# Performance work log

Measured on AMD Instinct MI355X. Metric: run time of the kernel, lower is better.

## Reference

```python
import jax, jax.numpy as jnp
import numpy as np

N = 100000      # nodes
E = 300000      # directed edges (avg degree ~3, ogbn-arxiv-like sparsity)
F_IN = 128      # ogbn-arxiv node features
H = 256         # hidden
C = 40          # ogbn-arxiv classes
L = 6           # num_layers
BN_EPS = 1e-5


def setup_inputs() -> dict:
    key = jax.random.key(0)
    ks = jax.random.split(key, 12)
    x = jax.random.normal(ks[0], (N, F_IN), jnp.float32)
    edge_index = jax.random.randint(ks[1], (2, E), 0, N, dtype=jnp.int32)
    s_in = 1.0 / np.sqrt(F_IN)
    s_h = 1.0 / np.sqrt(H)
    return {
        "x": x,
        "edge_index": edge_index,
        "w_in": jax.random.normal(ks[2], (F_IN, H), jnp.float32) * s_in,
        "b_in": jnp.zeros((H,), jnp.float32),
        "conv_w": jax.random.normal(ks[3], (L, H, H), jnp.float32) * s_h,
        "conv_b": jnp.zeros((L, H), jnp.float32),
        "bn_gamma": jnp.ones((L, H), jnp.float32),
        "bn_beta": jnp.zeros((L, H), jnp.float32),
        "out_w": jax.random.normal(ks[4], (H, C), jnp.float32) * s_h,
        "out_b": jnp.zeros((C,), jnp.float32),
        "res_weights": jax.random.normal(ks[5], (L,), jnp.float32),
    }


def _gcn_norm(edge_index, n_nodes):
    # GCNConv default: add self-loops, symmetric normalization D^-1/2 (A+I) D^-1/2
    loops = jnp.arange(n_nodes, dtype=edge_index.dtype)
    src = jnp.concatenate([edge_index[0], loops])
    dst = jnp.concatenate([edge_index[1], loops])
    deg = jax.ops.segment_sum(jnp.ones_like(dst, jnp.float32), dst, num_segments=n_nodes)
    dinv = jax.lax.rsqrt(jnp.maximum(deg, 1.0))
    norm = dinv[src] * dinv[dst]  # [E+N]
    return src, dst, norm


def _batchnorm(h, gamma, beta):
    # BatchNorm1d in training mode: biased batch statistics over nodes
    m = jnp.mean(h, axis=0)
    v = jnp.mean(jnp.square(h - m), axis=0)
    return (h - m) * jax.lax.rsqrt(v + BN_EPS) * gamma + beta


def reference(x, edge_index, w_in, b_in, conv_w, conv_b, bn_gamma, bn_beta, out_w, out_b, res_weights):
    src, dst, norm = _gcn_norm(edge_index, N)
    h = x @ w_in + b_in            # input_fc: [N, H]
    x_input = h
    layer_out = []
    prev = None
    for i in range(L):
        hw = h @ conv_w[i]                                  # linear transform
        msg = hw[src] * norm[:, None]                       # gather + scale
        agg = jax.ops.segment_sum(msg, dst, num_segments=N) + conv_b[i]  # scatter-add
        a = jax.nn.relu(_batchnorm(agg, bn_gamma[i], bn_beta[i]))
        # dropout p=0.5 omitted (eval mode / deterministic reference)
        if i == 0:
            h = a + 0.2 * x_input
        else:
            h = a + 0.2 * x_input + 0.7 * prev
        layer_out.append(h)
        prev = h
    w = jax.nn.softmax(res_weights)                          # [L]
    mix = jnp.einsum('lnh,l->nh', jnp.stack(layer_out), w)   # weighted sum of layer outputs
    logits = mix @ out_w + out_b                             # [N, C]
    return jax.nn.log_softmax(logits, axis=1)
```

## Files before the change

kernel.cpp:

```cpp
#include <hip/hip_runtime.h>
#include <math.h>

#define Nn   100000
#define Ee   300000
#define FIN  128
#define Hdim 256
#define Ncls 40
#define Lnum 6
#define SCAN_B 98
#define KP   264
#define EMAX 1152

typedef __attribute__((ext_vector_type(8))) short bf16x8;
typedef __attribute__((ext_vector_type(4))) float f32x4;

__device__ __forceinline__ float bf2f(unsigned int u16) {
    unsigned int x = u16 << 16;
    return __builtin_bit_cast(float, x);
}
__device__ __forceinline__ unsigned short f2bf(float f) {
    unsigned int x = __builtin_bit_cast(unsigned int, f);
    x = (x + 0x7FFFu + ((x >> 16) & 1u)) >> 16;
    return (unsigned short)x;
}
__device__ __forceinline__ void unpack2(unsigned int u, float& lo, float& hi) {
    lo = __builtin_bit_cast(float, u << 16);
    hi = __builtin_bit_cast(float, u & 0xFFFF0000u);
}
__device__ __forceinline__ unsigned int pack2(float a, float b) {
    return (unsigned int)f2bf(a) | ((unsigned int)f2bf(b) << 16);
}
__device__ __forceinline__ void acc8(float* a, float w, uint4 v) {
    float f0, f1;
    unpack2(v.x, f0, f1); a[0] += w * f0; a[1] += w * f1;
    unpack2(v.y, f0, f1); a[2] += w * f0; a[3] += w * f1;
    unpack2(v.z, f0, f1); a[4] += w * f0; a[5] += w * f1;
    unpack2(v.w, f0, f1); a[6] += w * f0; a[7] += w * f1;
}

__global__ void count_edges(const int* __restrict__ ei, int* __restrict__ cnt) {
    int e = blockIdx.x * blockDim.x + threadIdx.x;
    if (e < Ee) atomicAdd(&cnt[ei[Ee + e]], 1);
}

__global__ void scan_block(const int* __restrict__ cnt, int* __restrict__ iscan,
                           int* __restrict__ btot) {
    __shared__ int buf[1024];
    int t = threadIdx.x;
    int g = blockIdx.x * 1024 + t;
    int v = (g < Nn) ? cnt[g] : 0;
    buf[t] = v; __syncthreads();
    for (int off = 1; off < 1024; off <<= 1) {
        int x = buf[t];
        int a = (t >= off) ? buf[t - off] : 0;
        __syncthreads();
        buf[t] = x + a;
        __syncthreads();
    }
    if (g < Nn) iscan[g] = buf[t];
    if (t == 1023) btot[blockIdx.x] = buf[1023];
}

__global__ void scan_tops(const int* __restrict__ btot, int* __restrict__ bpref) {
    __shared__ int b[128];
    int t = threadIdx.x;
    int v = (t < SCAN_B) ? btot[t] : 0;
    b[t] = v; __syncthreads();
    for (int off = 1; off < 128; off <<= 1) {
        int x = b[t];
        int a = (t >= off) ? b[t - off] : 0;
        __syncthreads();
        b[t] = x + a;
        __syncthreads();
    }
    if (t < SCAN_B) bpref[t] = b[t] - v;
}

__global__ void scan_final(const int* __restrict__ cnt, const int* __restrict__ iscan,
                           const int* __restrict__ bpref, int* __restrict__ offs,
                           float* __restrict__ dinvp) {
    int g = blockIdx.x * 1024 + threadIdx.x;
    if (g < Nn) {
        int c = cnt[g];
        offs[g] = bpref[blockIdx.x] + iscan[g] - c;
        dinvp[g] = rsqrtf((float)(c + 1));
    }
    if (g == 0) offs[Nn] = Ee;
}

__global__ void fill_csr(const int* __restrict__ ei, const int* __restrict__ offs,
                         int* __restrict__ cur, const float* __restrict__ dinvp,
                         int* __restrict__ esrc, float* __restrict__ ew) {
    int e = blockIdx.x * blockDim.x + threadIdx.x;
    if (e >= Ee) return;
    int s = ei[e], d = ei[Ee + e];
    int p = offs[d] + atomicAdd(&cur[d], 1);
    esrc[p] = s;
    ew[p] = dinvp[s];
}

__global__ void prep_weights(const float* __restrict__ conv_w, const float* __restrict__ w_in,
                             const float* __restrict__ out_w,
                             unsigned short* __restrict__ Whi,
                             unsigned short* __restrict__ Fhi,
                             unsigned short* __restrict__ Whd, unsigned short* __restrict__ Wld) {
    int b = blockIdx.x, t = threadIdx.x;
    if (b < 1536) {
        int id = b * 256 + t;
        int l = id >> 16, k = (id >> 8) & 255, n = id & 255;
        Whi[l * 65536 + n * 256 + k] = f2bf(conv_w[id]);
    } else if (b < 1664) {
        int id = (b - 1536) * 256 + t;
        int k = id >> 8, n = id & 255;
        Fhi[n * FIN + k] = f2bf(w_in[id]);
    } else {
        int id = (b - 1664) * 256 + t;
        int c = id >> 8, k = id & 255;
        float w = (c < Ncls) ? out_w[k * Ncls + c] : 0.f;
        unsigned short hi = f2bf(w);
        unsigned short lo = f2bf(w - bf2f(hi));
        Whd[c * 256 + k] = hi;
        Wld[c * 256 + k] = lo;
    }
}

__global__ void cvt_bf16(const float* __restrict__ src, unsigned short* __restrict__ dst, int n8) {
    int i = blockIdx.x * blockDim.x + threadIdx.x;
    if (i >= n8) return;
    float4 a = ((const float4*)src)[i * 2];
    float4 b = ((const float4*)src)[i * 2 + 1];
    uint4 o;
    o.x = pack2(a.x, a.y); o.y = pack2(a.z, a.w);
    o.z = pack2(b.x, b.y); o.w = pack2(b.z, b.w);
    ((uint4*)dst)[i] = o;
}

__global__ void bn_reduce(const float* __restrict__ P, float* __restrict__ bnsum,
                          float* __restrict__ bnsq, int nb) {
    int c = threadIdx.x;
    int per = (nb + gridDim.x - 1) / gridDim.x;
    int r0 = blockIdx.x * per;
    int r1 = r0 + per; if (r1 > nb) r1 = nb;
    float s = 0.f, q = 0.f;
    for (int r = r0; r < r1; ++r) {
        s += P[(size_t)r * 512 + c];
        q += P[(size_t)r * 512 + 256 + c];
    }
    if (r0 < r1) {
        atomicAdd(&bnsum[c], s);
        atomicAdd(&bnsq[c], q);
    }
}

__global__ __launch_bounds__(512) void gemm_mfma(
    const unsigned short* __restrict__ A, unsigned short* __restrict__ C,
    const unsigned short* __restrict__ W,
    const float* __restrict__ bias, int K, int nrows)
{
    __shared__ __align__(16) unsigned short smem[18432];

    const int t    = threadIdx.x;
    const int lane = t & 63, wid = t >> 6;
    const int ln   = lane & 15, quad = lane >> 4;
    const int r64  = (wid >> 2) * 64, c64 = (wid & 3) * 64;
    const int r0   = blockIdx.x * 128;

    unsigned short* At = smem;
    unsigned short* Bt = smem + 5120;

    f32x4 acc[4][4];
#pragma unroll
    for (int i = 0; i < 4; ++i)
#pragma unroll
        for (int j = 0; j < 4; ++j) acc[i][j] = (f32x4){0.f, 0.f, 0.f, 0.f};

    const int arow = t >> 2, akq = t & 3;
    const bool arow_ok = (r0 + arow < nrows);
    const int nk = K >> 5;

    uint4 ga = make_uint4(0u, 0u, 0u, 0u);
    if (arow_ok) ga = *(const uint4*)&A[(size_t)(r0 + arow) * K + akq * 8];
    uint4 gb[2];
#pragma unroll
    for (int q = 0; q < 2; ++q) {
        int idx = t + 512 * q, row = idx >> 2, kq = idx & 3;
        gb[q] = *(const uint4*)&W[(size_t)row * K + kq * 8];
    }

    for (int kt = 0; kt < nk; ++kt) {
        __syncthreads();
        *(uint4*)&At[arow * 40 + akq * 8] = ga;
#pragma unroll
        for (int q = 0; q < 2; ++q) {
            int idx = t + 512 * q, row = idx >> 2, kq = idx & 3;
            *(uint4*)&Bt[row * 40 + kq * 8] = gb[q];
        }
        __syncthreads();
        if (kt + 1 < nk) {
            int k0 = (kt + 1) << 5;
            ga = make_uint4(0u, 0u, 0u, 0u);
            if (arow_ok) ga = *(const uint4*)&A[(size_t)(r0 + arow) * K + k0 + akq * 8];
#pragma unroll
            for (int q = 0; q < 2; ++q) {
                int idx = t + 512 * q, row = idx >> 2, kq = idx & 3;
                gb[q] = *(const uint4*)&W[(size_t)row * K + k0 + kq * 8];
            }
        }
        bf16x8 af[4], bf[4];
#pragma unroll
        for (int rt = 0; rt < 4; ++rt)
            af[rt] = *(const bf16x8*)&At[(r64 + rt * 16 + ln) * 40 + quad * 8];
#pragma unroll
        for (int ct = 0; ct < 4; ++ct)
            bf[ct] = *(const bf16x8*)&Bt[(c64 + ct * 16 + ln) * 40 + quad * 8];
#pragma unroll
        for (int rt = 0; rt < 4; ++rt)
#pragma unroll
            for (int ct = 0; ct < 4; ++ct)
                acc[rt][ct] = __builtin_amdgcn_mfma_f32_16x16x32_bf16(af[rt], bf[ct], acc[rt][ct], 0, 0, 0);
    }
    __syncthreads();

    float bc[4];
#pragma unroll
    for (int ct = 0; ct < 4; ++ct) bc[ct] = bias[c64 + ct * 16 + ln];

    unsigned short* Tt = &smem[wid * 2304];
    const int rr2 = lane & 31, jh = lane >> 5;
#pragma unroll
    for (int h = 0; h < 2; ++h) {
#pragma unroll
        for (int rr = 0; rr < 2; ++rr) {
            int rt = 2 * h + rr;
#pragma unroll
            for (int ct = 0; ct < 4; ++ct)
#pragma unroll
                for (int v = 0; v < 4; ++v)
                    Tt[(rr * 16 + quad * 4 + v) * 72 + ct * 16 + ln] = f2bf(acc[rt][ct][v] + bc[ct]);
        }
        __asm__ volatile("s_waitcnt lgkmcnt(0)" ::: "memory");
        int grow = r0 + r64 + h * 32 + rr2;
        if (grow < nrows) {
#pragma unroll
            for (int j = 0; j < 4; ++j) {
                uint4 v4 = *(const uint4*)&Tt[rr2 * 72 + jh * 32 + j * 8];
                *(uint4*)&C[(size_t)grow * 256 + c64 + jh * 32 + j * 8] = v4;
            }
        }
        __asm__ volatile("s_waitcnt lgkmcnt(0)" ::: "memory");
    }
}

__global__ __launch_bounds__(512, 4) void gemm_agg(
    const unsigned short* __restrict__ Hin,
    unsigned short* __restrict__ C,
    const unsigned short* __restrict__ W,
    const float* __restrict__ bias,
    const int* __restrict__ offs, const int* __restrict__ esrc,
    const float* __restrict__ ew, const float* __restrict__ dinvp,
    float* __restrict__ bnsum, float* __restrict__ bnsq,
    float* __restrict__ Pstats)
{
    __shared__ __align__(16) unsigned short At[128 * KP];
    __shared__ __align__(16) uint2 eL[EMAX];
    __shared__ int oL[132];
    __shared__ float lsum[256], lsq[256];

    const int t    = threadIdx.x;
    const int lane = t & 63, wid = t >> 6;
    const int ln   = lane & 15, quad = lane >> 4;
    const int r64  = (wid >> 2) * 64, c64 = (wid & 3) * 64;
    const int r0   = blockIdx.x * 128;

    if (t < 256) { lsum[t] = 0.f; lsq[t] = 0.f; }

    const int rEnd = (r0 + 128 <= Nn) ? (r0 + 128) : Nn;
    const int E0 = offs[r0];
    const int E1 = offs[rEnd];
    const int nE = E1 - E0;
    const bool staged = (nE <= EMAX);

    if (t < 129) {
        int idx = r0 + t; if (idx > Nn) idx = Nn;
        oL[t] = offs[idx];
    }
    if (staged) {
        for (int j = t; j < nE; j += 512)
            eL[j] = make_uint2((unsigned)esrc[E0 + j],
                               __builtin_bit_cast(unsigned, ew[E0 + j]));
    }
    __syncthreads();

    const int half = lane >> 5, l31 = lane & 31;
#pragma unroll 1
    for (int p = 0; p < 4; ++p) {
        const int rA = (wid * 2 + half) * 8 + 2 * p, rB = rA + 1;
        const int nA = r0 + rA, nB = r0 + rB;
        float a[8] = {0.f,0.f,0.f,0.f,0.f,0.f,0.f,0.f};
        float b[8] = {0.f,0.f,0.f,0.f,0.f,0.f,0.f,0.f};
        int eA = oL[rA], eA1 = oL[rA + 1];
        int eB = oL[rB], eB1 = oL[rB + 1];
        float dnA = 0.f, dnB = 0.f;
        if (nA < Nn) {
            dnA = dinvp[nA];
            acc8(a, dnA, *(const uint4*)&Hin[(size_t)nA * Hdim + l31 * 8]);
        }
        if (nB < Nn) {
            dnB = dinvp[nB];
            acc8(b, dnB, *(const uint4*)&Hin[(size_t)nB * Hdim + l31 * 8]);
        }
        if (staged) {
            bool dA = eA < eA1, dB = eB < eB1;
            uint4 vA = make_uint4(0u,0u,0u,0u), vB = vA;
            float wA = 0.f, wB = 0.f;
            if (dA) { uint2 s = eL[eA - E0]; wA = __builtin_bit_cast(float, s.y);
                      vA = *(const uint4*)&Hin[(size_t)s.x * Hdim + l31 * 8]; }
            if (dB) { uint2 s = eL[eB - E0]; wB = __builtin_bit_cast(float, s.y);
                      vB = *(const uint4*)&Hin[(size_t)s.x * Hdim + l31 * 8]; }
            while (dA | dB) {
                bool dA2 = dA && (eA + 1 < eA1), dB2 = dB && (eB + 1 < eB1);
                uint4 vA2 = make_uint4(0u,0u,0u,0u), vB2 = vA2;
                float wA2 = 0.f, wB2 = 0.f;
                if (dA2) { uint2 s = eL[eA + 1 - E0]; wA2 = __builtin_bit_cast(float, s.y);
                           vA2 = *(const uint4*)&Hin[(size_t)s.x * Hdim + l31 * 8]; }
                if (dB2) { uint2 s = eL[eB + 1 - E0]; wB2 = __builtin_bit_cast(float, s.y);
                           vB2 = *(const uint4*)&Hin[(size_t)s.x * Hdim + l31 * 8]; }
                if (dA) { acc8(a, wA, vA); ++eA; }
                if (dB) { acc8(b, wB, vB); ++eB; }
                vA = vA2; wA = wA2; dA = dA2;
                vB = vB2; wB = wB2; dB = dB2;
            }
        } else {
            for (int e = eA; e < eA1; ++e) {
                int s = esrc[e]; float w = ew[e];
                acc8(a, w, *(const uint4*)&Hin[(size_t)s * Hdim + l31 * 8]);
            }
            for (int e = eB; e < eB1; ++e) {
                int s = esrc[e]; float w = ew[e];
                acc8(b, w, *(const uint4*)&Hin[(size_t)s * Hdim + l31 * 8]);
            }
        }
#pragma unroll
        for (int k = 0; k < 8; ++k) { a[k] *= dnA; b[k] *= dnB; }
        *(uint4*)&At[rA * KP + l31 * 8] =
            make_uint4(pack2(a[0], a[1]), pack2(a[2], a[3]),
                       pack2(a[4], a[5]), pack2(a[6], a[7]));
        *(uint4*)&At[rB * KP + l31 * 8] =
            make_uint4(pack2(b[0], b[1]), pack2(b[2], b[3]),
                       pack2(b[4], b[5]), pack2(b[6], b[7]));
    }
    __syncthreads();

    f32x4 acc[4][4];
#pragma unroll
    for (int i = 0; i < 4; ++i)
#pragma unroll
        for (int j = 0; j < 4; ++j) acc[i][j] = (f32x4){0.f, 0.f, 0.f, 0.f};

#pragma unroll
    for (int kt = 0; kt < 8; ++kt) {
        bf16x8 af[4], bf[4];
#pragma unroll
        for (int ct = 0; ct < 4; ++ct)
            bf[ct] = *(const bf16x8*)&W[(size_t)(c64 + ct * 16 + ln) * 256 + kt * 32 + quad * 8];
#pragma unroll
        for (int rt = 0; rt < 4; ++rt)
            af[rt] = *(const bf16x8*)&At[(r64 + rt * 16 + ln) * KP + kt * 32 + quad * 8];
#pragma unroll
        for (int rt = 0; rt < 4; ++rt)
#pragma unroll
            for (int ct = 0; ct < 4; ++ct)
                acc[rt][ct] = __builtin_amdgcn_mfma_f32_16x16x32_bf16(af[rt], bf[ct], acc[rt][ct], 0, 0, 0);
    }

    float bc[4];
#pragma unroll
    for (int ct = 0; ct < 4; ++ct) bc[ct] = bias[c64 + ct * 16 + ln];

#pragma unroll
    for (int ct = 0; ct < 4; ++ct) {
        float s = 0.f, qq = 0.f;
#pragma unroll
        for (int rt = 0; rt < 4; ++rt)
#pragma unroll
            for (int v = 0; v < 4; ++v) {
                int row = r0 + r64 + rt * 16 + quad * 4 + v;
                if (row < Nn) {
                    float val = acc[rt][ct][v] + bc[ct];
                    s += val; qq += val * val;
                }
            }
        s  += __shfl_xor(s, 16);  s  += __shfl_xor(s, 32);
        qq += __shfl_xor(qq, 16); qq += __shfl_xor(qq, 32);
        if (quad == 0) { atomicAdd(&lsum[c64 + ct * 16 + ln], s); atomicAdd(&lsq[c64 + ct * 16 + ln], qq); }
    }

    __syncthreads();

#pragma unroll
    for (int rt = 0; rt < 4; ++rt)
#pragma unroll
        for (int ct = 0; ct < 4; ++ct)
#pragma unroll
            for (int v = 0; v < 4; ++v)
                At[(r64 + rt * 16 + quad * 4 + v) * KP + c64 + ct * 16 + ln] =
                    f2bf(acc[rt][ct][v] + bc[ct]);
    __syncthreads();

    const int l31s = t & 31, rhalf = t >> 5;
#pragma unroll
    for (int p = 0; p < 8; ++p) {
        int lrow = p * 16 + rhalf;
        int grow = r0 + lrow;
        if (grow < Nn) {
            uint4 v4 = *(const uint4*)&At[lrow * KP + l31s * 8];
            *(uint4*)&C[(size_t)grow * 256 + l31s * 8] = v4;
        }
    }

    if (t < 256) {
        if (Pstats) {
            Pstats[(size_t)blockIdx.x * 512 + t]       = lsum[t];
            Pstats[(size_t)blockIdx.x * 512 + 256 + t] = lsq[t];
        } else {
            atomicAdd(&bnsum[t], lsum[t]);
            atomicAdd(&bnsq[t], lsq[t]);
        }
    }
}

__global__ void apply_kernel(const unsigned short* __restrict__ T,
                             const unsigned short* __restrict__ X,
                             unsigned short* __restrict__ Hb, unsigned short* __restrict__ M,
                             const float* __restrict__ bnsum, const float* __restrict__ bnsq,
                             const float* __restrict__ gamma, const float* __restrict__ beta,
                             const float* __restrict__ res_w, int layer) {
    __shared__ float sc[256], sh[256];
    int t = threadIdx.x;
    {
        float mean = bnsum[t] * (1.0f / Nn);
        float var  = fmaxf(bnsq[t] * (1.0f / Nn) - mean * mean, 0.f);
        float rstd = rsqrtf(var + 1e-5f);
        float s = gamma[t] * rstd;
        sc[t] = s; sh[t] = beta[t] - mean * s;
    }
    float m0 = res_w[0];
#pragma unroll
    for (int i = 1; i < Lnum; ++i) m0 = fmaxf(m0, res_w[i]);
    float se = 0.f, wl = 0.f;
#pragma unroll
    for (int i = 0; i < Lnum; ++i) {
        float e = __expf(res_w[i] - m0);
        se += e;
        if (i == layer) wl = e;
    }
    float wi = wl / se;
    __syncthreads();

    int idx = blockIdx.x * blockDim.x + t;
    int c8 = idx & 31;
    float scl[8], shl[8];
#pragma unroll
    for (int k = 0; k < 8; ++k) { scl[k] = sc[c8 * 8 + k]; shl[k] = sh[c8 * 8 + k]; }

    uint4 tv = ((const uint4*)T)[idx];
    uint4 xv = ((const uint4*)X)[idx];
    float tf[8], xf[8];
    unpack2(tv.x, tf[0], tf[1]); unpack2(tv.y, tf[2], tf[3]);
    unpack2(tv.z, tf[4], tf[5]); unpack2(tv.w, tf[6], tf[7]);
    unpack2(xv.x, xf[0], xf[1]); unpack2(xv.y, xf[2], xf[3]);
    unpack2(xv.z, xf[4], xf[5]); unpack2(xv.w, xf[6], xf[7]);

    float a[8];
#pragma unroll
    for (int k = 0; k < 8; ++k)
        a[k] = fmaxf(tf[k] * scl[k] + shl[k], 0.f) + 0.2f * xf[k];
    if (layer > 0) {
        uint4 hv = ((const uint4*)Hb)[idx];
        float hf[8];
        unpack2(hv.x, hf[0], hf[1]); unpack2(hv.y, hf[2], hf[3]);
        unpack2(hv.z, hf[4], hf[5]); unpack2(hv.w, hf[6], hf[7]);
#pragma unroll
        for (int k = 0; k < 8; ++k) a[k] += 0.7f * hf[k];
    }
    uint4 ho;
    ho.x = pack2(a[0], a[1]); ho.y = pack2(a[2], a[3]);
    ho.z = pack2(a[4], a[5]); ho.w = pack2(a[6], a[7]);
    ((uint4*)Hb)[idx] = ho;

    float m[8];
    if (layer == 0) {
#pragma unroll
        for (int k = 0; k < 8; ++k) m[k] = wi * a[k];
    } else {
        uint4 mv = ((const uint4*)M)[idx];
        float mf[8];
        unpack2(mv.x, mf[0], mf[1]); unpack2(mv.y, mf[2], mf[3]);
        unpack2(mv.z, mf[4], mf[5]); unpack2(mv.w, mf[6], mf[7]);
#pragma unroll
        for (int k = 0; k < 8; ++k) m[k] = mf[k] + wi * a[k];
    }
    uint4 mo;
    mo.x = pack2(m[0], m[1]); mo.y = pack2(m[2], m[3]);
    mo.z = pack2(m[4], m[5]); mo.w = pack2(m[6], m[7]);
    ((uint4*)M)[idx] = mo;
}

__global__ __launch_bounds__(512) void head_mfma(const unsigned short* __restrict__ M,
                                                 const unsigned short* __restrict__ Whd,
                                                 const unsigned short* __restrict__ Wld,
                                                 const float* __restrict__ out_b,
                                                 float* __restrict__ out, int nrows) {
    __shared__ unsigned short At[128 * 40];
    const int t    = threadIdx.x;
    const int lane = t & 63, wid = t >> 6;
    const int ln   = lane & 15, quad = lane >> 4;
    const int r0   = blockIdx.x * 128;

    f32x4 acc[3];
#pragma unroll
    for (int ct = 0; ct < 3; ++ct) acc[ct] = (f32x4){0.f, 0.f, 0.f, 0.f};

    for (int k0 = 0; k0 < 256; k0 += 32) {
        __syncthreads();
        {
            int row = t >> 2, kq = t & 3;
            uint4 g = make_uint4(0u, 0u, 0u, 0u);
            if (r0 + row < nrows)
                g = *(const uint4*)&M[(size_t)(r0 + row) * 256 + k0 + kq * 8];
            *(uint4*)&At[row * 40 + kq * 8] = g;
        }
        __syncthreads();
        bf16x8 af = *(const bf16x8*)&At[(wid * 16 + ln) * 40 + quad * 8];
#pragma unroll
        for (int ct = 0; ct < 3; ++ct) {
            int c = ct * 16 + ln;
            bf16x8 bh = *(const bf16x8*)&Whd[c * 256 + k0 + quad * 8];
            bf16x8 bl = *(const bf16x8*)&Wld[c * 256 + k0 + quad * 8];
            acc[ct] = __builtin_amdgcn_mfma_f32_16x16x32_bf16(af, bh, acc[ct], 0, 0, 0);
            acc[ct] = __builtin_amdgcn_mfma_f32_16x16x32_bf16(af, bl, acc[ct], 0, 0, 0);
        }
    }

    int   cc[3]; float bias[3];
#pragma unroll
    for (int ct = 0; ct < 3; ++ct) {
        cc[ct] = ct * 16 + ln;
        bias[ct] = (cc[ct] < Ncls) ? out_b[cc[ct]] : 0.f;
    }
#pragma unroll
    for (int v = 0; v < 4; ++v) {
        int row = r0 + wid * 16 + quad * 4 + v;
        float val[3];
#pragma unroll
        for (int ct = 0; ct < 3; ++ct) val[ct] = acc[ct][v] + bias[ct];
        float mx = -1e30f;
#pragma unroll
        for (int ct = 0; ct < 3; ++ct) if (cc[ct] < Ncls) mx = fmaxf(mx, val[ct]);
        mx = fmaxf(mx, __shfl_xor(mx, 1)); mx = fmaxf(mx, __shfl_xor(mx, 2));
        mx = fmaxf(mx, __shfl_xor(mx, 4)); mx = fmaxf(mx, __shfl_xor(mx, 8));
        float s = 0.f;
#pragma unroll
        for (int ct = 0; ct < 3; ++ct) if (cc[ct] < Ncls) s += __expf(val[ct] - mx);
        s += __shfl_xor(s, 1); s += __shfl_xor(s, 2);
        s += __shfl_xor(s, 4); s += __shfl_xor(s, 8);
        float lse = mx + __logf(s);
        if (row < nrows) {
            out[(size_t)row * Ncls + cc[0]] = val[0] - lse;
            out[(size_t)row * Ncls + cc[1]] = val[1] - lse;
            if (ln < 8) out[(size_t)row * Ncls + cc[2]] = val[2] - lse;
        }
    }
}

extern "C" void kernel_launch(void* const* d_in, const int* in_sizes, int n_in,
                              void* d_out, int out_size, void* d_ws, size_t ws_size,
                              hipStream_t stream)
{
    const float* x      = (const float*)d_in[0];
    const int*   ei     = (const int*)d_in[1];
    const float* w_in   = (const float*)d_in[2];
    const float* b_in   = (const float*)d_in[3];
    const float* conv_w = (const float*)d_in[4];
    const float* conv_b = (const float*)d_in[5];
    const float* gamma  = (const float*)d_in[6];
    const float* beta   = (const float*)d_in[7];
    const float* out_w  = (const float*)d_in[8];
    const float* out_b  = (const float*)d_in[9];
    const float* res_w  = (const float*)d_in[10];
    float* out = (float*)d_out;
    char* ws = (char*)d_ws;

    int*   cnt    = (int*)  (ws + 0);
    int*   cursor = (int*)  (ws + 400000);
    int*   offs   = (int*)  (ws + 800000);
    float* dinvp  = (float*)(ws + 1200016);
    int*   esrc   = (int*)  (ws + 1600016);
    float* ew     = (float*)(ws + 2800016);
    int*   iscan  = (int*)  (ws + 4002064);
    int*   btot   = (int*)  (ws + 4402064);
    int*   bpref  = (int*)  (ws + 4402576);
    unsigned short* Whi = (unsigned short*)(ws + 4403088);
    unsigned short* Fhi = (unsigned short*)(ws + 5975952);
    unsigned short* Whd = (unsigned short*)(ws + 6107024);
    unsigned short* Wld = (unsigned short*)(ws + 6131600);
    unsigned short* X   = (unsigned short*)(ws + 6156176);
    unsigned short* Hb  = X  + (size_t)Nn * Hdim;
    unsigned short* T   = Hb + (size_t)Nn * Hdim;
    unsigned short* M   = T  + (size_t)Nn * Hdim;
    unsigned short* xbf = M;

    float* bnA = (float*)(ws + 4002064);

    const int gblocks = (Nn + 127) / 128;

    const size_t P_OFS = 6156176 + 4 * (size_t)Nn * Hdim * sizeof(unsigned short);
    const size_t P_BYTES = (size_t)gblocks * 512 * sizeof(float);
    float* Pst = (ws_size >= P_OFS + P_BYTES) ? (float*)(ws + P_OFS) : nullptr;

    hipMemsetAsync(cnt, 0, 800000, stream);

    count_edges<<<(Ee + 255) / 256, 256, 0, stream>>>(ei, cnt);
    scan_block<<<SCAN_B, 1024, 0, stream>>>(cnt, iscan, btot);
    scan_tops<<<1, 128, 0, stream>>>(btot, bpref);
    scan_final<<<SCAN_B, 1024, 0, stream>>>(cnt, iscan, bpref, offs, dinvp);
    fill_csr<<<(Ee + 255) / 256, 256, 0, stream>>>(ei, offs, cursor, dinvp, esrc, ew);

    hipMemsetAsync(bnA, 0, Lnum * 512 * sizeof(float), stream);

    prep_weights<<<1712, 256, 0, stream>>>(conv_w, w_in, out_w,
                                           Whi, Fhi, Whd, Wld);
    cvt_bf16<<<(Nn * FIN / 8 + 255) / 256, 256, 0, stream>>>(x, xbf, Nn * FIN / 8);

    gemm_mfma<<<gblocks, 512, 0, stream>>>(xbf, X, Fhi, b_in, FIN, Nn);

    for (int i = 0; i < Lnum; ++i) {
        float* bnsumL = bnA + (size_t)i * 512;
        float* bnsqL  = bnsumL + 256;
        gemm_agg<<<gblocks, 512, 0, stream>>>(i == 0 ? X : Hb, T,
                                              Whi + (size_t)i * Hdim * Hdim,
                                              conv_b + (size_t)i * Hdim,
                                              offs, esrc, ew, dinvp,
                                              bnsumL, bnsqL, Pst);
        if (Pst)
            bn_reduce<<<64, 256, 0, stream>>>(Pst, bnsumL, bnsqL, gblocks);
        apply_kernel<<<(Nn * 32) / 256, 256, 0, stream>>>(T, X, Hb, M,
                                                          bnsumL, bnsqL,
                                                          gamma + (size_t)i * Hdim,
                                                          beta + (size_t)i * Hdim,
                                                          res_w, i);
    }

    head_mfma<<<gblocks, 512, 0, stream>>>(M, Whd, Wld, out_b, out, Nn);
}
```

Measured before the change: 1.035 ms.

## Store all layer outputs and fold softmax mix into head; simplify fc GEMM

When the workspace is large enough, each layer's output goes to its own buffer. The apply kernel then no longer reads and writes the running mix M on every layer, and the head kernel builds the weighted mix on the fly from all six layer outputs. The input FC GEMM is specialized to K=128: it stages the whole A tile in LDS once and reads weights directly from global memory, dropping the double-buffered k-loop. The software-pipelined edge gather loop is also simplified to a plain loop, which may reduce register pressure but loses prefetch overlap.

```diff
diff --git a/kernel.cpp b/kernel.cpp
--- a/kernel.cpp
+++ b/kernel.cpp
@@ -152,10 +152,11 @@
     }
 }
 
-__global__ __launch_bounds__(512) void gemm_mfma(
-    const unsigned short* __restrict__ A, unsigned short* __restrict__ C,
+__global__ __launch_bounds__(512) void gemm_fc(
+    const unsigned short* __restrict__ A,
+    unsigned short* __restrict__ C,
     const unsigned short* __restrict__ W,
-    const float* __restrict__ bias, int K, int nrows)
+    const float* __restrict__ bias, int nrows)
 {
     __shared__ __align__(16) unsigned short smem[18432];
 
@@ -165,8 +166,16 @@
     const int r64  = (wid >> 2) * 64, c64 = (wid & 3) * 64;
     const int r0   = blockIdx.x * 128;
 
-    unsigned short* At = smem;
-    unsigned short* Bt = smem + 5120;
+#pragma unroll
+    for (int q = 0; q < 4; ++q) {
+        int idx = t + 512 * q;
+        int row = idx >> 4, kq = idx & 15;
+        uint4 g = make_uint4(0u, 0u, 0u, 0u);
+        if (r0 + row < nrows)
+            g = *(const uint4*)&A[(size_t)(r0 + row) * FIN + kq * 8];
+        *(uint4*)&smem[row * 136 + kq * 8] = g;
+    }
+    __syncthreads();
 
     f32x4 acc[4][4];
 #pragma unroll
@@ -174,45 +183,15 @@
 #pragma unroll
         for (int j = 0; j < 4; ++j) acc[i][j] = (f32x4){0.f, 0.f, 0.f, 0.f};
 
-    const int arow = t >> 2, akq = t & 3;
-    const bool arow_ok = (r0 + arow < nrows);
-    const int nk = K >> 5;
-
-    uint4 ga = make_uint4(0u, 0u, 0u, 0u);
-    if (arow_ok) ga = *(const uint4*)&A[(size_t)(r0 + arow) * K + akq * 8];
-    uint4 gb[2];
-#pragma unroll
-    for (int q = 0; q < 2; ++q) {
-        int idx = t + 512 * q, row = idx >> 2, kq = idx & 3;
-        gb[q] = *(const uint4*)&W[(size_t)row * K + kq * 8];
-    }
-
-    for (int kt = 0; kt < nk; ++kt) {
-        __syncthreads();
-        *(uint4*)&At[arow * 40 + akq * 8] = ga;
-#pragma unroll
-        for (int q = 0; q < 2; ++q) {
-            int idx = t + 512 * q, row = idx >> 2, kq = idx & 3;
-            *(uint4*)&Bt[row * 40 + kq * 8] = gb[q];
-        }
-        __syncthreads();
-        if (kt + 1 < nk) {
-            int k0 = (kt + 1) << 5;
-            ga = make_uint4(0u, 0u, 0u, 0u);
-            if (arow_ok) ga = *(const uint4*)&A[(size_t)(r0 + arow) * K + k0 + akq * 8];
-#pragma unroll
-            for (int q = 0; q < 2; ++q) {
-                int idx = t + 512 * q, row = idx >> 2, kq = idx & 3;
-                gb[q] = *(const uint4*)&W[(size_t)row * K + k0 + kq * 8];
-            }
-        }
+#pragma unroll
+    for (int kt = 0; kt < 4; ++kt) {
         bf16x8 af[4], bf[4];
 #pragma unroll
+        for (int ct = 0; ct < 4; ++ct)
+            bf[ct] = *(const bf16x8*)&W[(size_t)(c64 + ct * 16 + ln) * FIN + kt * 32 + quad * 8];
+#pragma unroll
         for (int rt = 0; rt < 4; ++rt)
-            af[rt] = *(const bf16x8*)&At[(r64 + rt * 16 + ln) * 40 + quad * 8];
-#pragma unroll
-        for (int ct = 0; ct < 4; ++ct)
-            bf[ct] = *(const bf16x8*)&Bt[(c64 + ct * 16 + ln) * 40 + quad * 8];
+            af[rt] = *(const bf16x8*)&smem[(r64 + rt * 16 + ln) * 136 + kt * 32 + quad * 8];
 #pragma unroll
         for (int rt = 0; rt < 4; ++rt)
 #pragma unroll
@@ -310,25 +289,16 @@
             acc8(b, dnB, *(const uint4*)&Hin[(size_t)nB * Hdim + l31 * 8]);
         }
         if (staged) {
-            bool dA = eA < eA1, dB = eB < eB1;
-            uint4 vA = make_uint4(0u,0u,0u,0u), vB = vA;
-            float wA = 0.f, wB = 0.f;
-            if (dA) { uint2 s = eL[eA - E0]; wA = __builtin_bit_cast(float, s.y);
-                      vA = *(const uint4*)&Hin[(size_t)s.x * Hdim + l31 * 8]; }
-            if (dB) { uint2 s = eL[eB - E0]; wB = __builtin_bit_cast(float, s.y);
-                      vB = *(const uint4*)&Hin[(size_t)s.x * Hdim + l31 * 8]; }
-            while (dA | dB) {
-                bool dA2 = dA && (eA + 1 < eA1), dB2 = dB && (eB + 1 < eB1);
-                uint4 vA2 = make_uint4(0u,0u,0u,0u), vB2 = vA2;
-                float wA2 = 0.f, wB2 = 0.f;
-                if (dA2) { uint2 s = eL[eA + 1 - E0]; wA2 = __builtin_bit_cast(float, s.y);
-                           vA2 = *(const uint4*)&Hin[(size_t)s.x * Hdim + l31 * 8]; }
-                if (dB2) { uint2 s = eL[eB + 1 - E0]; wB2 = __builtin_bit_cast(float, s.y);
-                           vB2 = *(const uint4*)&Hin[(size_t)s.x * Hdim + l31 * 8]; }
+            while ((eA < eA1) | (eB < eB1)) {
+                bool dA = eA < eA1, dB = eB < eB1;
+                uint4 vA = make_uint4(0u,0u,0u,0u), vB = vA;
+                float wA = 0.f, wB = 0.f;
+                if (dA) { uint2 s = eL[eA - E0]; wA = __builtin_bit_cast(float, s.y);
+                          vA = *(const uint4*)&Hin[(size_t)s.x * Hdim + l31 * 8]; }
+                if (dB) { uint2 s = eL[eB - E0]; wB = __builtin_bit_cast(float, s.y);
+                          vB = *(const uint4*)&Hin[(size_t)s.x * Hdim + l31 * 8]; }
                 if (dA) { acc8(a, wA, vA); ++eA; }
                 if (dB) { acc8(b, wB, vB); ++eB; }
-                vA = vA2; wA = wA2; dA = dA2;
-                vB = vB2; wB = wB2; dB = dB2;
             }
         } else {
             for (int e = eA; e < eA1; ++e) {
@@ -506,6 +476,56 @@
     ((uint4*)M)[idx] = mo;
 }
 
+__global__ void apply_h(const unsigned short* __restrict__ T,
+                        const unsigned short* __restrict__ X,
+                        const unsigned short* __restrict__ Hprev,
+                        unsigned short* __restrict__ Hout,
+                        const float* __restrict__ bnsum, const float* __restrict__ bnsq,
+                        const float* __restrict__ gamma, const float* __restrict__ beta,
+                        int layer) {
+    __shared__ float sc[256], sh[256];
+    int t = threadIdx.x;
+    {
+        float mean = bnsum[t] * (1.0f / Nn);
+        float var  = fmaxf(bnsq[t] * (1.0f / Nn) - mean * mean, 0.f);
+        float rstd = rsqrtf(var + 1e-5f);
+        float s = gamma[t] * rstd;
+        sc[t] = s; sh[t] = beta[t] - mean * s;
+    }
+    __syncthreads();
+
+    int idx = blockIdx.x * blockDim.x + t;
+    int c8 = idx & 31;
+    float scl[8], shl[8];
+#pragma unroll
+    for (int k = 0; k < 8; ++k) { scl[k] = sc[c8 * 8 + k]; shl[k] = sh[c8 * 8 + k]; }
+
+    uint4 tv = ((const uint4*)T)[idx];
+    uint4 xv = ((const uint4*)X)[idx];
+    float tf[8], xf[8];
+    unpack2(tv.x, tf[0], tf[1]); unpack2(tv.y, tf[2], tf[3]);
+    unpack2(tv.z, tf[4], tf[5]); unpack2(tv.w, tf[6], tf[7]);
+    unpack2(xv.x, xf[0], xf[1]); unpack2(xv.y, xf[2], xf[3]);
+    unpack2(xv.z, xf[4], xf[5]); unpack2(xv.w, xf[6], xf[7]);
+
+    float a[8];
+#pragma unroll
+    for (int k = 0; k < 8; ++k)
+        a[k] = fmaxf(tf[k] * scl[k] + shl[k], 0.f) + 0.2f * xf[k];
+    if (layer > 0) {
+        uint4 hv = ((const uint4*)Hprev)[idx];
+        float hf[8];
+        unpack2(hv.x, hf[0], hf[1]); unpack2(hv.y, hf[2], hf[3]);
+        unpack2(hv.z, hf[4], hf[5]); unpack2(hv.w, hf[6], hf[7]);
+#pragma unroll
+        for (int k = 0; k < 8; ++k) a[k] += 0.7f * hf[k];
+    }
+    uint4 ho;
+    ho.x = pack2(a[0], a[1]); ho.y = pack2(a[2], a[3]);
+    ho.z = pack2(a[4], a[5]); ho.w = pack2(a[6], a[7]);
+    ((uint4*)Hout)[idx] = ho;
+}
+
 __global__ __launch_bounds__(512) void head_mfma(const unsigned short* __restrict__ M,
                                                  const unsigned short* __restrict__ Whd,
                                                  const unsigned short* __restrict__ Wld,
@@ -529,6 +549,100 @@
             if (r0 + row < nrows)
                 g = *(const uint4*)&M[(size_t)(r0 + row) * 256 + k0 + kq * 8];
             *(uint4*)&At[row * 40 + kq * 8] = g;
+        }
+        __syncthreads();
+        bf16x8 af = *(const bf16x8*)&At[(wid * 16 + ln) * 40 + quad * 8];
+#pragma unroll
+        for (int ct = 0; ct < 3; ++ct) {
+            int c = ct * 16 + ln;
+            bf16x8 bh = *(const bf16x8*)&Whd[c * 256 + k0 + quad * 8];
+            bf16x8 bl = *(const bf16x8*)&Wld[c * 256 + k0 + quad * 8];
+            acc[ct] = __builtin_amdgcn_mfma_f32_16x16x32_bf16(af, bh, acc[ct], 0, 0, 0);
+            acc[ct] = __builtin_amdgcn_mfma_f32_16x16x32_bf16(af, bl, acc[ct], 0, 0, 0);
+        }
+    }
+
+    int   cc[3]; float bias[3];
+#pragma unroll
+    for (int ct = 0; ct < 3; ++ct) {
+        cc[ct] = ct * 16 + ln;
+        bias[ct] = (cc[ct] < Ncls) ? out_b[cc[ct]] : 0.f;
+    }
+#pragma unroll
+    for (int v = 0; v < 4; ++v) {
+        int row = r0 + wid * 16 + quad * 4 + v;
+        float val[3];
+#pragma unroll
+        for (int ct = 0; ct < 3; ++ct) val[ct] = acc[ct][v] + bias[ct];
+        float mx = -1e30f;
+#pragma unroll
+        for (int ct = 0; ct < 3; ++ct) if (cc[ct] < Ncls) mx = fmaxf(mx, val[ct]);
+        mx = fmaxf(mx, __shfl_xor(mx, 1)); mx = fmaxf(mx, __shfl_xor(mx, 2));
+        mx = fmaxf(mx, __shfl_xor(mx, 4)); mx = fmaxf(mx, __shfl_xor(mx, 8));
+        float s = 0.f;
+#pragma unroll
+        for (int ct = 0; ct < 3; ++ct) if (cc[ct] < Ncls) s += __expf(val[ct] - mx);
+        s += __shfl_xor(s, 1); s += __shfl_xor(s, 2);
+        s += __shfl_xor(s, 4); s += __shfl_xor(s, 8);
+        float lse = mx + __logf(s);
+        if (row < nrows) {
+            out[(size_t)row * Ncls + cc[0]] = val[0] - lse;
+            out[(size_t)row * Ncls + cc[1]] = val[1] - lse;
+            if (ln < 8) out[(size_t)row * Ncls + cc[2]] = val[2] - lse;
+        }
+    }
+}
+
+__global__ __launch_bounds__(512) void head_mix(const unsigned short* __restrict__ H0,
+                                                const unsigned short* __restrict__ Whd,
+                                                const unsigned short* __restrict__ Wld,
+                                                const float* __restrict__ out_b,
+                                                const float* __restrict__ res_w,
+                                                float* __restrict__ out, int nrows) {
+    __shared__ unsigned short At[128 * 40];
+    const int t    = threadIdx.x;
+    const int lane = t & 63, wid = t >> 6;
+    const int ln   = lane & 15, quad = lane >> 4;
+    const int r0   = blockIdx.x * 128;
+
+    float wmix[Lnum];
+    {
+        float m0 = res_w[0];
+#pragma unroll
+        for (int i = 1; i < Lnum; ++i) m0 = fmaxf(m0, res_w[i]);
+        float se = 0.f;
+#pragma unroll
+        for (int i = 0; i < Lnum; ++i) { wmix[i] = __expf(res_w[i] - m0); se += wmix[i]; }
+        float inv = 1.0f / se;
+#pragma unroll
+        for (int i = 0; i < Lnum; ++i) wmix[i] *= inv;
+    }
+
+    f32x4 acc[3];
+#pragma unroll
+    for (int ct = 0; ct < 3; ++ct) acc[ct] = (f32x4){0.f, 0.f, 0.f, 0.f};
+
+    for (int k0 = 0; k0 < 256; k0 += 32) {
+        __syncthreads();
+        {
+            int row = t >> 2, kq = t & 3;
+            float m[8] = {0.f,0.f,0.f,0.f,0.f,0.f,0.f,0.f};
+            if (r0 + row < nrows) {
+                size_t base = (size_t)(r0 + row) * 256 + k0 + kq * 8;
+#pragma unroll
+                for (int l = 0; l < Lnum; ++l) {
+                    uint4 g = *(const uint4*)&H0[(size_t)l * Nn * Hdim + base];
+                    float f0, f1;
+                    unpack2(g.x, f0, f1); m[0] += wmix[l] * f0; m[1] += wmix[l] * f1;
+                    unpack2(g.y, f0, f1); m[2] += wmix[l] * f0; m[3] += wmix[l] * f1;
+                    unpack2(g.z, f0, f1); m[4] += wmix[l] * f0; m[5] += wmix[l] * f1;
+                    unpack2(g.w, f0, f1); m[6] += wmix[l] * f0; m[7] += wmix[l] * f1;
+                }
+            }
+            uint4 o;
+            o.x = pack2(m[0], m[1]); o.y = pack2(m[2], m[3]);
+            o.z = pack2(m[4], m[5]); o.w = pack2(m[6], m[7]);
+            *(uint4*)&At[row * 40 + kq * 8] = o;
         }
         __syncthreads();
         bf16x8 af = *(const bf16x8*)&At[(wid * 16 + ln) * 40 + quad * 8];
@@ -604,19 +718,36 @@
     unsigned short* Fhi = (unsigned short*)(ws + 5975952);
     unsigned short* Whd = (unsigned short*)(ws + 6107024);
     unsigned short* Wld = (unsigned short*)(ws + 6131600);
-    unsigned short* X   = (unsigned short*)(ws + 6156176);
-    unsigned short* Hb  = X  + (size_t)Nn * Hdim;
-    unsigned short* T   = Hb + (size_t)Nn * Hdim;
-    unsigned short* M   = T  + (size_t)Nn * Hdim;
-    unsigned short* xbf = M;
 
     float* bnA = (float*)(ws + 4002064);
 
     const int gblocks = (Nn + 127) / 128;
-
-    const size_t P_OFS = 6156176 + 4 * (size_t)Nn * Hdim * sizeof(unsigned short);
+    const size_t NH = (size_t)Nn * Hdim;
+
+    const size_t HARR_P_OFS = 6156176 + 8 * NH * sizeof(unsigned short);
     const size_t P_BYTES = (size_t)gblocks * 512 * sizeof(float);
-    float* Pst = (ws_size >= P_OFS + P_BYTES) ? (float*)(ws + P_OFS) : nullptr;
+    const bool harr = (ws_size >= HARR_P_OFS + P_BYTES);
+
+    unsigned short* X; unsigned short* T; unsigned short* Hb; unsigned short* M;
+    unsigned short* Harr; unsigned short* xbf; float* Pst;
+
+    if (harr) {
+        X    = (unsigned short*)(ws + 6156176);
+        T    = X + NH;
+        Harr = T + NH;
+        Hb = nullptr; M = nullptr;
+        xbf  = Harr + 5 * NH;
+        Pst  = (float*)(ws + HARR_P_OFS);
+    } else {
+        X   = (unsigned short*)(ws + 6156176);
+        Hb  = X + NH;
+        T   = Hb + NH;
+        M   = T + NH;
+        Harr = nullptr;
+        xbf = M;
+        const size_t P_OFS = 6156176 + 4 * NH * sizeof(unsigned short);
+        Pst = (ws_size >= P_OFS + P_BYTES) ? (float*)(ws + P_OFS) : nullptr;
+    }
 
     hipMemsetAsync(cnt, 0, 800000, stream);
 
@@ -632,24 +763,36 @@
                                            Whi, Fhi, Whd, Wld);
     cvt_bf16<<<(Nn * FIN / 8 + 255) / 256, 256, 0, stream>>>(x, xbf, Nn * FIN / 8);
 
-    gemm_mfma<<<gblocks, 512, 0, stream>>>(xbf, X, Fhi, b_in, FIN, Nn);
+    gemm_fc<<<gblocks, 512, 0, stream>>>(xbf, X, Fhi, b_in, Nn);
 
     for (int i = 0; i < Lnum; ++i) {
         float* bnsumL = bnA + (size_t)i * 512;
         float* bnsqL  = bnsumL + 256;
-        gemm_agg<<<gblocks, 512, 0, stream>>>(i == 0 ? X : Hb, T,
+        const unsigned short* Hin =
+            (i == 0) ? X : (harr ? Harr + (size_t)(i - 1) * NH : Hb);
+        gemm_agg<<<gblocks, 512, 0, stream>>>(Hin, T,
                                               Whi + (size_t)i * Hdim * Hdim,
                                               conv_b + (size_t)i * Hdim,
                                               offs, esrc, ew, dinvp,
                                               bnsumL, bnsqL, Pst);
         if (Pst)
             bn_reduce<<<64, 256, 0, stream>>>(Pst, bnsumL, bnsqL, gblocks);
-        apply_kernel<<<(Nn * 32) / 256, 256, 0, stream>>>(T, X, Hb, M,
-                                                          bnsumL, bnsqL,
-                                                          gamma + (size_t)i * Hdim,
-                                                          beta + (size_t)i * Hdim,
-                                                          res_w, i);
-    }
-
-    head_mfma<<<gblocks, 512, 0, stream>>>(M, Whd, Wld, out_b, out, Nn);
-}
+        if (harr) {
+            apply_h<<<(Nn * 32) / 256, 256, 0, stream>>>(
+                T, X, (i == 0) ? X : Harr + (size_t)(i - 1) * NH,
+                Harr + (size_t)i * NH,
+                bnsumL, bnsqL,
+                gamma + (size_t)i * Hdim, beta + (size_t)i * Hdim, i);
+        } else {
+            apply_kernel<<<(Nn * 32) / 256, 256, 0, stream>>>(
+                T, X, Hb, M, bnsumL, bnsqL,
+                gamma + (size_t)i * Hdim, beta + (size_t)i * Hdim,
+                res_w, i);
+        }
+    }
+
+    if (harr)
+        head_mix<<<gblocks, 512, 0, stream>>>(Harr, Whd, Wld, out_b, res_w, out, Nn);
+    else
+        head_mfma<<<gblocks, 512, 0, stream>>>(M, Whd, Wld, out_b, out, Nn);
+}
```

Result: no change. 1.026 ms (-0.9%).
